# Optimization experiments

Measured on AMD Instinct MI355X. Metric: run time of the kernel, lower is better.

## Reference

```python
import jax, jax.numpy as jnp
import numpy as np

EPS = 1e-5

def mish(x):
    return x * jnp.tanh(jnp.logaddexp(x, 0.0))

def instance_norm(x, gamma, beta):
    # x: (N, C, D, H, W); normalize per (N, C) over spatial dims
    mu = jnp.mean(x, axis=(2, 3, 4), keepdims=True)
    var = jnp.var(x, axis=(2, 3, 4), keepdims=True)
    xh = (x - mu) * jax.lax.rsqrt(var + EPS)
    return xh * gamma[None, :, None, None, None] + beta[None, :, None, None, None]

def conv3d(x, w, stride, padding):
    return jax.lax.conv_general_dilated(
        x, w, window_strides=(stride, stride, stride), padding=padding,
        dimension_numbers=('NCDHW', 'OIDHW', 'NCDHW'))

def pad_k(k, p):
    # center-pad kernel spatial dims up to 5x5x5
    return jnp.pad(k, ((0, 0), (0, 0), (p, p), (p, p), (p, p)))

def mode_conv(x, t, c5, c3, c1, a3, a5, gw, gb, gamma, beta):
    N = x.shape[0]
    Co = c5.shape[0]
    # gate: Linear(num_tasks -> 5*Co), softmax over the 5 experts
    g = jax.nn.softmax((t @ gw.T + gb).reshape(N, 5, Co), axis=1)  # (N,5,Co)
    pool3 = jnp.full((3, 3, 3), 1.0 / 27.0, x.dtype)
    pool5 = jnp.full((5, 5, 5), 1.0 / 125.0, x.dtype)
    experts = jnp.stack([
        c5,                      # conv5x5
        pad_k(c3, 1),            # conv3x3 padded to 5
        pad_k(c1, 2),            # conv1x1 padded to 5
        pad_k(a3 * pool3, 1),    # avg3x3: (Co,Ci,1,1,1)*(3,3,3) broadcast, padded
        a5 * pool5,              # avg5x5
    ], axis=0)                   # (5, Co, Ci, 5, 5, 5)
    # per-sample synthesized kernel
    w = jnp.einsum('eoidhw,neo->noidhw', experts, g)  # (N, Co, Ci, 5,5,5)
    # per-sample conv3d, padding 'same' (training branch of original)
    y = jax.vmap(lambda xi, wi: conv3d(xi[None], wi, 1, 'SAME')[0])(x, w)
    return mish(instance_norm(y, gamma, beta))

def setup_inputs() -> dict:
    key = jax.random.key(0)
    ks = jax.random.split(key, 32)
    N, Ci, Co, T = 2, 32, 64, 10
    D = H = W = 64
    f32 = jnp.float32
    def kconv(k, co, ci, ksz, fan):
        bound = float(np.sqrt(6.0 / ((1.0 + 5.0) * fan)))  # kaiming_uniform a=sqrt(5), fan_out
        return jax.random.uniform(k, (co, ci, ksz, ksz, ksz), f32, -bound, bound)
    inp = {}
    inp['x'] = jax.random.normal(ks[0], (N, Ci, D, H, W), f32)
    inp['t'] = jax.random.normal(ks[1], (N, T), f32)
    def layer(base, ci, co):
        p = {}
        p['conv5'] = kconv(ks[base + 0], co, ci, 5, co * 125)
        p['conv3'] = kconv(ks[base + 1], co, ci, 3, co * 27)
        p['conv1'] = kconv(ks[base + 2], co, ci, 1, co)
        p['avg3'] = kconv(ks[base + 3], co, ci, 1, co)
        p['avg5'] = kconv(ks[base + 4], co, ci, 1, co)
        gb_bound = 1.0 / np.sqrt(T)
        p['gw'] = jax.random.uniform(ks[base + 5], (5 * co, T), f32, -gb_bound, gb_bound)
        p['gb'] = jax.random.uniform(ks[base + 6], (5 * co,), f32, -gb_bound, gb_bound)
        p['gamma'] = jnp.ones((co,), f32)
        p['beta'] = jnp.zeros((co,), f32)
        return p
    for name, v in layer(2, Ci, Co).items():
        inp['l1_' + name] = v
    for name, v in layer(12, Co, Co).items():
        inp['l2_' + name] = v
    dw_bound = float(np.sqrt(1.0 / (Co * 8)))
    inp['down_w'] = jax.random.uniform(ks[25], (Co, Co, 2, 2, 2), f32, -dw_bound, dw_bound)
    inp['down_gamma'] = jnp.ones((Co,), f32)
    inp['down_beta'] = jnp.zeros((Co,), f32)
    return inp

def reference(x, t,
              l1_conv5, l1_conv3, l1_conv1, l1_avg3, l1_avg5, l1_gw, l1_gb, l1_gamma, l1_beta,
              l2_conv5, l2_conv3, l2_conv1, l2_avg3, l2_avg5, l2_gw, l2_gb, l2_gamma, l2_beta,
              down_w, down_gamma, down_beta):
    h = mode_conv(x, t, l1_conv5, l1_conv3, l1_conv1, l1_avg3, l1_avg5, l1_gw, l1_gb, l1_gamma, l1_beta)
    x_skip = mode_conv(h, t, l2_conv5, l2_conv3, l2_conv1, l2_avg3, l2_avg5, l2_gw, l2_gb, l2_gamma, l2_beta)
    y = conv3d(x_skip, down_w, 2, 'VALID')
    y = mish(instance_norm(y, down_gamma, down_beta))
    return (y, x_skip)
```

## Files before the change

kernel.cpp:

```cpp
#include <hip/hip_runtime.h>
#include <cstdint>
#include <cstddef>

constexpr int NB  = 2;
constexpr int CO  = 64;
constexpr int DIM = 64;
constexpr int SP  = DIM * DIM * DIM;
constexpr int NC  = NB * CO;
constexpr int Y_SZ = NB * CO * 32 * 32 * 32;

typedef float f32x4 __attribute__((ext_vector_type(4)));
typedef short s16x8 __attribute__((ext_vector_type(8)));

__device__ __forceinline__ unsigned short f2bf(float f) {
    unsigned int u = __float_as_uint(f);
    unsigned int r = (u + 0x7fffu + ((u >> 16) & 1u)) >> 16;
    return (unsigned short)r;
}
__device__ __forceinline__ float bf2f(unsigned short u) {
    return __uint_as_float((unsigned int)u << 16);
}
__device__ __forceinline__ unsigned int pack2(float a, float b) {
    return (unsigned int)f2bf(a) | ((unsigned int)f2bf(b) << 16);
}
__device__ __forceinline__ float mish_f(float x) {
    float e = __expf(x);
    float num = e * (e + 2.f);
    float r = x * num * __builtin_amdgcn_rcpf(num + 2.f);
    return (x > 15.f) ? x : r;
}

__device__ __forceinline__ void gload_lds16(const void* g, void* l) {
    __builtin_amdgcn_global_load_lds(
        (const __attribute__((address_space(1))) unsigned int*)g,
        (__attribute__((address_space(3))) unsigned int*)l, 16, 0, 0);
}

__global__ void gate2_kernel(const float* __restrict__ t,
                             const float* __restrict__ gw1, const float* __restrict__ gb1,
                             float* __restrict__ g1,
                             const float* __restrict__ gw2, const float* __restrict__ gb2,
                             float* __restrict__ g2,
                             float* __restrict__ zbuf) {
    int tid = threadIdx.x;
    if (tid < 64) zbuf[tid] = 0.f;
    int layer = tid >> 7;
    int lt = tid & 127;
    int n = lt >> 6, co = lt & 63;
    const float* gw = layer ? gw2 : gw1;
    const float* gb = layer ? gb2 : gb1;
    float* g = layer ? g2 : g1;
    float tl[10];
#pragma unroll
    for (int k = 0; k < 10; ++k) tl[k] = t[n * 10 + k];
    float l[5];
#pragma unroll
    for (int e = 0; e < 5; ++e) {
        int row = e * CO + co;
        float acc = gb[row];
#pragma unroll
        for (int k = 0; k < 10; ++k) acc += tl[k] * gw[row * 10 + k];
        l[e] = acc;
    }
    float m = l[0];
#pragma unroll
    for (int e = 1; e < 5; ++e) m = fmaxf(m, l[e]);
    float s = 0.f;
#pragma unroll
    for (int e = 0; e < 5; ++e) { l[e] = expf(l[e] - m); s += l[e]; }
    float inv = 1.f / s;
#pragma unroll
    for (int e = 0; e < 5; ++e) g[(n * 5 + e) * CO + co] = l[e] * inv;
}

template <int CI>
__device__ __forceinline__ void synth_one(int idx, const float* __restrict__ g,
                                          const float* __restrict__ c5, const float* __restrict__ c3,
                                          const float* __restrict__ c1, const float* __restrict__ a3,
                                          const float* __restrict__ a5,
                                          unsigned short* __restrict__ wbuf) {
    int tap = idx % 125;
    int ci  = (idx / 125) % CI;
    int co  = (idx / (125 * CI)) % CO;
    int n   = idx / (125 * CI * CO);
    const float* gn = g + n * 5 * CO;
    float g0 = gn[0 * CO + co], g1 = gn[1 * CO + co], g2 = gn[2 * CO + co],
          g3 = gn[3 * CO + co], g4 = gn[4 * CO + co];
    int dz = tap / 25, dy = (tap / 5) % 5, dx = tap % 5;
    int oc = co * CI + ci;
    float v = g0 * c5[(size_t)oc * 125 + tap] + g4 * a5[oc] * (1.f / 125.f);
    if (dz >= 1 && dz <= 3 && dy >= 1 && dy <= 3 && dx >= 1 && dx <= 3)
        v += g1 * c3[(size_t)oc * 27 + (dz - 1) * 9 + (dy - 1) * 3 + (dx - 1)]
           + g3 * a3[oc] * (1.f / 27.f);
    if (dz == 2 && dy == 2 && dx == 2) v += g2 * c1[oc];
    int t = (dy * 5 + dx);
    int cich = ci >> 5, cil = ci & 31;
    wbuf[((((size_t)(n * 5 + dz) * (CI / 32) + cich) * 25 + t) * 64 + co) * 32 + cil] = f2bf(v);
}

__global__ void synth2_kernel(const float* __restrict__ g1,
                              const float* __restrict__ c51, const float* __restrict__ c31,
                              const float* __restrict__ c11, const float* __restrict__ a31,
                              const float* __restrict__ a51, unsigned short* __restrict__ w1,
                              const float* __restrict__ g2,
                              const float* __restrict__ c52, const float* __restrict__ c32,
                              const float* __restrict__ c12, const float* __restrict__ a32,
                              const float* __restrict__ a52, unsigned short* __restrict__ w2) {
    constexpr int T1 = NB * CO * 32 * 125;
    constexpr int T2 = NB * CO * 64 * 125;
    int idx = blockIdx.x * 256 + threadIdx.x;
    if (idx < T1)
        synth_one<32>(idx, g1, c51, c31, c11, a31, a51, w1);
    else if (idx < T1 + T2)
        synth_one<64>(idx - T1, g2, c52, c32, c12, a32, a52, w2);
}

__global__ __launch_bounds__(256) void x_to_cl(const float* __restrict__ x,
                                               unsigned short* __restrict__ xcl) {
    __shared__ float ld[32][256];
    int b = blockIdx.x;
    int n = b >> 10;
    size_t base = (size_t)(b & 1023) * 256;
    int tid = threadIdx.x;
    const float* xp = x + (size_t)n * 32 * SP + base + tid;
#pragma unroll
    for (int c = 0; c < 32; ++c) ld[c][tid] = xp[(size_t)c * SP];
    __syncthreads();
    uint4* op = (uint4*)(xcl + ((size_t)n * SP + base) * 32);
#pragma unroll
    for (int r = 0; r < 4; ++r) {
        int idx = r * 256 + tid;
        int px = idx >> 2, q = idx & 3;
        uint4 o;
        o.x = pack2(ld[q * 8 + 0][px], ld[q * 8 + 1][px]);
        o.y = pack2(ld[q * 8 + 2][px], ld[q * 8 + 3][px]);
        o.z = pack2(ld[q * 8 + 4][px], ld[q * 8 + 5][px]);
        o.w = pack2(ld[q * 8 + 6][px], ld[q * 8 + 7][px]);
        op[idx] = o;
    }
}

template <int CI, int PCH, bool OUT_G8>
__global__ __launch_bounds__(512, 4) void conv5_mfma(const unsigned short* __restrict__ xin,
                                                     const unsigned short* __restrict__ wbuf,
                                                     unsigned short* __restrict__ outp,
                                                     float* __restrict__ part,
                                                     const void* __restrict__ zbuf) {
    constexpr int NCH = CI / 32;
    constexpr int NS  = 5 * NCH;
    __shared__ __align__(16) unsigned short lds[2][12800];

    const int bid = blockIdx.x;
    const int b   = (bid & 7) * 256 + (bid >> 3);
    const int xt  = b & 3;
    const int yt  = (b >> 2) & 3;
    const int z   = (b >> 4) & 63;
    const int n   = b >> 10;
    const int tid = threadIdx.x;
    const int lane = tid & 63, wv = tid >> 6;
    const int xl = lane & 15, kh = lane >> 4;
    const int yh = wv >> 2, cq = wv & 3;

    f32x4 acc[8];
#pragma unroll
    for (int pt = 0; pt < 8; ++pt)
#pragma unroll
        for (int j = 0; j < 4; ++j) acc[pt][j] = 0.f;

    long goff[4]; int gval[4];
#pragma unroll
    for (int r = 0; r < 4; ++r) {
        int idx = tid + r * 512;
        int p = idx >> 2, khs = idx & 3;
        int xx = p % 20, yy = p / 20;
        int yi = yt * 16 - 2 + yy, xi = xt * 16 - 2 + xx;
        gval[r] = ((unsigned)yi < 64u) && ((unsigned)xi < 64u);
        goff[r] = ((long)(yi * 64 + xi) * CI + khs * 8) * 2;
    }

    auto stage = [&](int s, int buf) {
        int dz = s / NCH, cich = s % NCH;
        int zi = z + dz - 2;
        bool zok = (unsigned)zi < 64u;
        const char* pb = (const char*)xin
                       + ((size_t)(n * SP + zi * 4096) * CI + cich * 32) * 2;
        char* lb = (char*)&lds[buf][0];
#pragma unroll
        for (int r = 0; r < 4; ++r) {
            int idx = tid + r * 512;
            if (idx < 1600) {
                const void* g = (zok && gval[r]) ? (const void*)(pb + goff[r]) : zbuf;
                gload_lds16(g, lb + idx * 16);
            }
        }
    };

    auto compute = [&](int s, int buf) {
        int dz = s / NCH, cich = s % NCH;
        const unsigned short* wp = wbuf
            + ((size_t)((n * 5 + dz) * NCH + cich) * 25) * 2048
            + cq * 512 + xl * 32 + kh * 8;
        const char* src = (const char*)&lds[buf][0];
        __builtin_amdgcn_s_setprio(1);
#pragma unroll 1
        for (int dx = 0; dx < 5; ++dx) {
            int xx = xl + dx;
            s16x8 fr[12];
#pragma unroll
            for (int r = 0; r < 12; ++r) {
                int row = yh * 8 + r;
                fr[r] = *(const s16x8*)(src + (size_t)(row * 20 + xx) * 64 + kh * 16);
            }
#pragma unroll
            for (int dy = 0; dy < 5; ++dy) {
                s16x8 a = *(const s16x8*)(wp + (size_t)(dy * 5 + dx) * 2048);
#pragma unroll
                for (int pt = 0; pt < 8; ++pt)
                    acc[pt] = __builtin_amdgcn_mfma_f32_16x16x32_bf16(
                        a, fr[pt + dy], acc[pt], 0, 0, 0);
            }
        }
        __builtin_amdgcn_s_setprio(0);
    };

    stage(0, 0);
    __syncthreads();
#pragma unroll 1
    for (int s = 0; s < NS; ++s) {
        if (s + 1 < NS) stage(s + 1, (s + 1) & 1);
        compute(s, s & 1);
        __syncthreads();
    }

    {
        float s1[4], s2[4];
#pragma unroll
        for (int j = 0; j < 4; ++j) { s1[j] = 0.f; s2[j] = 0.f; }
#pragma unroll
        for (int pt = 0; pt < 8; ++pt)
#pragma unroll
            for (int j = 0; j < 4; ++j) {
                float v = acc[pt][j];
                s1[j] += v; s2[j] += v * v;
            }
#pragma unroll
        for (int o = 1; o < 16; o <<= 1)
#pragma unroll
            for (int j = 0; j < 4; ++j) {
                s1[j] += __shfl_xor(s1[j], o, 64);
                s2[j] += __shfl_xor(s2[j], o, 64);
            }
        if (xl == 0) {
            int co = cq * 16 + kh * 4;
            int cb = (b & 1023) * 2 + yh;
#pragma unroll
            for (int j = 0; j < 4; ++j) {
                part[((size_t)(n * 2 + 0) * 64 + co + j) * PCH + cb] = s1[j];
                part[((size_t)(n * 2 + 1) * 64 + co + j) * PCH + cb] = s2[j];
            }
        }
    }

    {
        char* tb = (char*)&lds[0][0];
#pragma unroll
        for (int pt = 0; pt < 8; ++pt) {
            int pix = (yh * 8 + pt) * 16 + xl;
            unsigned int ad = ((unsigned)(pix * 128 + cq * 32 + kh * 8))
                              ^ ((unsigned)(pix & 7) << 4);
            *(unsigned int*)(tb + ad)     = pack2(acc[pt][0], acc[pt][1]);
            *(unsigned int*)(tb + ad + 4) = pack2(acc[pt][2], acc[pt][3]);
        }
        __syncthreads();
#pragma unroll
        for (int it = 0; it < 4; ++it) {
            int idx = it * 512 + tid;
            int pix = idx >> 3, ch = idx & 7;
            uint4 v = *(const uint4*)(tb + (((unsigned)idx * 16)
                                            ^ ((unsigned)(pix & 7) << 4)));
            int y = yt * 16 + (pix >> 4), x = xt * 16 + (pix & 15);
            size_t zyx = (size_t)z * 4096 + y * 64 + x;
            if (OUT_G8)
                *(uint4*)(outp + ((size_t)(n * 8 + ch) * SP + zyx) * 8) = v;
            else
                *(uint4*)(outp + ((size_t)n * SP + zyx) * 64 + ch * 8) = v;
        }
    }
}

template <int CH>
__global__ void stats_fin(const float* __restrict__ part, float* __restrict__ st,
                          float invS) {
    int blk = blockIdx.x;
    int n = blk >> 6, co = blk & 63;
    int tid = threadIdx.x;
    const float* ps = part + ((size_t)(n * 2 + 0) * 64 + co) * CH;
    const float* pq = part + ((size_t)(n * 2 + 1) * 64 + co) * CH;
    float s1 = 0.f, s2 = 0.f;
    for (int i = tid; i < CH; i += 256) { s1 += ps[i]; s2 += pq[i]; }
#pragma unroll
    for (int o = 1; o < 64; o <<= 1) {
        s1 += __shfl_xor(s1, o, 64);
        s2 += __shfl_xor(s2, o, 64);
    }
    __shared__ float sh1[4], sh2[4];
    if ((tid & 63) == 0) { sh1[tid >> 6] = s1; sh2[tid >> 6] = s2; }
    __syncthreads();
    if (tid == 0) {
        float a = sh1[0] + sh1[1] + sh1[2] + sh1[3];
        float q = sh2[0] + sh2[1] + sh2[2] + sh2[3];
        float mean = a * invS;
        float var  = q * invS - mean * mean;
        st[(n * 64 + co) * 2]     = mean;
        st[(n * 64 + co) * 2 + 1] = rsqrtf(var + 1e-5f);
    }
}

__global__ void norm_mish_cl_kernel(unsigned short* __restrict__ h,
                                    const float* __restrict__ st,
                                    const float* __restrict__ gamma,
                                    const float* __restrict__ beta) {
    size_t idx = (size_t)blockIdx.x * 256 + threadIdx.x;
    uint4 v = ((uint4*)h)[idx];
    int c0 = ((int)(idx & 7)) * 8;
    size_t pix = idx >> 3;
    int n = (int)(pix >> 18);
    unsigned int* pv = &v.x;
#pragma unroll
    for (int q = 0; q < 4; ++q) {
        unsigned int wv = pv[q];
        unsigned int out = 0;
#pragma unroll
        for (int hv = 0; hv < 2; ++hv) {
            int c = c0 + 2 * q + hv;
            int nc = n * 64 + c;
            float val = bf2f((unsigned short)((wv >> (16 * hv)) & 0xffffu));
            float xh = (val - st[nc * 2]) * st[nc * 2 + 1] * gamma[c] + beta[c];
            out |= ((unsigned int)f2bf(mish_f(xh))) << (16 * hv);
        }
        pv[q] = out;
    }
    ((uint4*)h)[idx] = v;
}

template <int SHIFT>
__global__ void norm_mish_kernel(float* __restrict__ buf, const float* __restrict__ stats,
                                 const float* __restrict__ gamma, const float* __restrict__ beta,
                                 int total4) {
    int idx = blockIdx.x * 256 + threadIdx.x;
    if (idx >= total4) return;
    float4 v = reinterpret_cast<float4*>(buf)[idx];
    int nc = idx >> (SHIFT - 2);
    int c  = nc & 63;
    float mean = stats[nc * 2], inv = stats[nc * 2 + 1];
    float ga = gamma[c], be = beta[c];
    float* pv = &v.x;
#pragma unroll
    for (int k = 0; k < 4; ++k) {
        float xh = (pv[k] - mean) * inv * ga + be;
        pv[k] = mish_f(xh);
    }
    reinterpret_cast<float4*>(buf)[idx] = v;
}

__global__ __launch_bounds__(256) void down_conv_kernel(const unsigned short* __restrict__ h3,
                                                        const float* __restrict__ dw,
                                                        const float* __restrict__ st,
                                                        const float* __restrict__ gamma,
                                                        const float* __restrict__ beta,
                                                        float* __restrict__ xskip,
                                                        float* __restrict__ out,
                                                        float* __restrict__ part) {
    __shared__ float ls[8][2][8][64];
    int b   = blockIdx.x;
    int yt  = b & 7;
    int z   = (b >> 3) & 31;
    int n   = b >> 8;
    int tid = threadIdx.x;
    int xo  = tid & 31;
    int cog = tid >> 5;

    float acc[4][8];
#pragma unroll
    for (int yo = 0; yo < 4; ++yo)
#pragma unroll
        for (int j = 0; j < 8; ++j) acc[yo][j] = 0.f;

    for (int cc = 0; cc < 8; ++cc) {
#pragma unroll
        for (int r = 0; r < 4; ++r) {
            int p  = r * 256 + tid;
            int xx = p & 63, yy = (p >> 6) & 7, dz = p >> 9;
            int zi = 2 * z + dz, yi = yt * 8 + yy;
            size_t zyx = (size_t)zi * 4096 + yi * 64 + xx;
            uint4 v = *(const uint4*)(h3 + ((size_t)(n * 8 + cc) * SP + zyx) * 8);
            unsigned int* pv = &v.x;
#pragma unroll
            for (int q = 0; q < 4; ++q) {
#pragma unroll
                for (int hv = 0; hv < 2; ++hv) {
                    int c  = 2 * q + hv;
                    int ci = cc * 8 + c;
                    int nc = n * 64 + ci;
                    float val = bf2f((unsigned short)((pv[q] >> (16 * hv)) & 0xffffu));
                    float nv  = mish_f((val - st[nc * 2]) * st[nc * 2 + 1] * gamma[ci]
                                       + beta[ci]);
                    ls[c][dz][yy][xx] = nv;
                    xskip[((size_t)(n * CO + ci) * 64 + zi) * 4096 + yi * 64 + xx] = nv;
                }
            }
        }
        __syncthreads();
#pragma unroll 1
        for (int c = 0; c < 8; ++c) {
            int ci = cc * 8 + c;
#pragma unroll
            for (int tap = 0; tap < 8; ++tap) {
                int dz = tap >> 2, dy = (tap >> 1) & 1, dx = tap & 1;
                float w[8];
#pragma unroll
                for (int j = 0; j < 8; ++j)
                    w[j] = dw[((size_t)(cog * 8 + j) * CO + ci) * 8 + tap];
#pragma unroll
                for (int yo = 0; yo < 4; ++yo) {
                    float xv = ls[c][dz][yo * 2 + dy][2 * xo + dx];
#pragma unroll
                    for (int j = 0; j < 8; ++j) acc[yo][j] += w[j] * xv;
                }
            }
        }
        __syncthreads();
    }
#pragma unroll
    for (int yo = 0; yo < 4; ++yo)
#pragma unroll
        for (int j = 0; j < 8; ++j)
            out[((size_t)(n * CO + cog * 8 + j) * 32 + z) * 1024 + (yt * 4 + yo) * 32 + xo]
                = acc[yo][j];

    float s1[8], s2[8];
#pragma unroll
    for (int j = 0; j < 8; ++j) { s1[j] = 0.f; s2[j] = 0.f; }
#pragma unroll
    for (int yo = 0; yo < 4; ++yo)
#pragma unroll
        for (int j = 0; j < 8; ++j) {
            float v = acc[yo][j];
            s1[j] += v; s2[j] += v * v;
        }
#pragma unroll
    for (int o = 1; o < 32; o <<= 1)
#pragma unroll
        for (int j = 0; j < 8; ++j) {
            s1[j] += __shfl_xor(s1[j], o, 64);
            s2[j] += __shfl_xor(s2[j], o, 64);
        }
    if (xo == 0) {
        int cb = b & 255;
#pragma unroll
        for (int j = 0; j < 8; ++j) {
            int co = cog * 8 + j;
            part[((size_t)(n * 2 + 0) * 64 + co) * 256 + cb] = s1[j];
            part[((size_t)(n * 2 + 1) * 64 + co) * 256 + cb] = s2[j];
        }
    }
}

extern "C" void kernel_launch(void* const* d_in, const int* in_sizes, int n_in,
                              void* d_out, int out_size, void* d_ws, size_t ws_size,
                              hipStream_t stream) {
    const float* x      = (const float*)d_in[0];
    const float* t      = (const float*)d_in[1];
    const float* l1_c5  = (const float*)d_in[2];
    const float* l1_c3  = (const float*)d_in[3];
    const float* l1_c1  = (const float*)d_in[4];
    const float* l1_a3  = (const float*)d_in[5];
    const float* l1_a5  = (const float*)d_in[6];
    const float* l1_gw  = (const float*)d_in[7];
    const float* l1_gb  = (const float*)d_in[8];
    const float* l1_ga  = (const float*)d_in[9];
    const float* l1_be  = (const float*)d_in[10];
    const float* l2_c5  = (const float*)d_in[11];
    const float* l2_c3  = (const float*)d_in[12];
    const float* l2_c1  = (const float*)d_in[13];
    const float* l2_a3  = (const float*)d_in[14];
    const float* l2_a5  = (const float*)d_in[15];
    const float* l2_gw  = (const float*)d_in[16];
    const float* l2_gb  = (const float*)d_in[17];
    const float* l2_ga  = (const float*)d_in[18];
    const float* l2_be  = (const float*)d_in[19];
    const float* down_w = (const float*)d_in[20];
    const float* dn_ga  = (const float*)d_in[21];
    const float* dn_be  = (const float*)d_in[22];

    char* ws = (char*)d_ws;
    unsigned short* xcl = (unsigned short*)(ws);
    unsigned short* h3  = (unsigned short*)(ws);
    float* part1 = (float*)(ws + 33554432);
    unsigned short* h2  = (unsigned short*)(ws + 67108864);
    unsigned short* w1  = (unsigned short*)(ws + 134217728);
    unsigned short* w2  = (unsigned short*)(ws + 135241728);
    float* part2 = (float*)(ws + 137289728);
    float* part3 = (float*)(ws + 139386880);
    float* g1    = (float*)(ws + 139649024);
    float* g2    = (float*)(ws + 139651584);
    float* st1   = (float*)(ws + 139654144);
    float* st2   = (float*)(ws + 139655168);
    float* st3   = (float*)(ws + 139656192);
    float* zbuf  = (float*)(ws + 139657216);

    float* yout  = (float*)d_out;
    float* xskip = (float*)d_out + Y_SZ;

    gate2_kernel<<<1, 256, 0, stream>>>(t, l1_gw, l1_gb, g1, l2_gw, l2_gb, g2, zbuf);
    synth2_kernel<<<6000, 256, 0, stream>>>(g1, l1_c5, l1_c3, l1_c1, l1_a3, l1_a5, w1,
                                            g2, l2_c5, l2_c3, l2_c1, l2_a3, l2_a5, w2);
    x_to_cl<<<2048, 256, 0, stream>>>(x, xcl);

    conv5_mfma<32, 2048, false><<<2048, 512, 0, stream>>>(xcl, w1, h2, part1, zbuf);
    stats_fin<2048><<<128, 256, 0, stream>>>(part1, st1, 1.f / SP);
    norm_mish_cl_kernel<<<16384, 256, 0, stream>>>(h2, st1, l1_ga, l1_be);

    conv5_mfma<64, 2048, true><<<2048, 512, 0, stream>>>(h2, w2, h3, part2, zbuf);
    stats_fin<2048><<<128, 256, 0, stream>>>(part2, st2, 1.f / SP);

    down_conv_kernel<<<NB * 32 * 8, 256, 0, stream>>>(h3, down_w, st2, l2_ga, l2_be,
                                                      xskip, yout, part3);
    stats_fin<256><<<128, 256, 0, stream>>>(part3, st3, 1.f / 32768.f);
    norm_mish_kernel<15><<<(NC * 32768 / 4 + 255) / 256, 256, 0, stream>>>(
        yout, st3, dn_ga, dn_be, NC * 32768 / 4);
}
```

Measured before the change: 758.4 us.

## Switch conv5 to 32x32x16 MFMA with 8x32 spatial tiles and LDS stats

Replaces the 16x16x32 bf16 MFMA conv with 32x32x16 MFMA tiles, changing the block's spatial tile from 16x16 to 8 rows by 32 columns and reorganizing the LDS staging layout and fragment loads to match. Each wave now computes 32 channels by 2 rows of 32 pixels, reducing fragment loads per MFMA and weight register traffic. Instance-norm partial statistics are now computed from the bf16-rounded values staged in LDS with a block-level reduction, giving one partial per block and halving the stats_fin input. The stats change rounding slightly and the larger LDS footprint may affect occupancy.

```diff
diff --git a/kernel.cpp b/kernel.cpp
--- a/kernel.cpp
+++ b/kernel.cpp
@@ -9,8 +9,9 @@
 constexpr int NC  = NB * CO;
 constexpr int Y_SZ = NB * CO * 32 * 32 * 32;
 
-typedef float f32x4 __attribute__((ext_vector_type(4)));
-typedef short s16x8 __attribute__((ext_vector_type(8)));
+typedef float f32x4  __attribute__((ext_vector_type(4)));
+typedef float f32x16 __attribute__((ext_vector_type(16)));
+typedef short s16x8  __attribute__((ext_vector_type(8)));
 
 __device__ __forceinline__ unsigned short f2bf(float f) {
     unsigned int u = __float_as_uint(f);
@@ -141,41 +142,43 @@
 }
 
 template <int CI, int PCH, bool OUT_G8>
-__global__ __launch_bounds__(512, 4) void conv5_mfma(const unsigned short* __restrict__ xin,
-                                                     const unsigned short* __restrict__ wbuf,
-                                                     unsigned short* __restrict__ outp,
-                                                     float* __restrict__ part,
-                                                     const void* __restrict__ zbuf) {
+__global__ __launch_bounds__(512, 4) void conv5_mfma32(const unsigned short* __restrict__ xin,
+                                                       const unsigned short* __restrict__ wbuf,
+                                                       unsigned short* __restrict__ outp,
+                                                       float* __restrict__ part,
+                                                       const void* __restrict__ zbuf) {
     constexpr int NCH = CI / 32;
     constexpr int NS  = 5 * NCH;
-    __shared__ __align__(16) unsigned short lds[2][12800];
+    __shared__ __align__(16) unsigned short lds[2][13824];
 
     const int bid = blockIdx.x;
     const int b   = (bid & 7) * 256 + (bid >> 3);
-    const int xt  = b & 3;
-    const int yt  = (b >> 2) & 3;
+    const int xt  = b & 1;
+    const int yt  = (b >> 1) & 7;
     const int z   = (b >> 4) & 63;
     const int n   = b >> 10;
     const int tid = threadIdx.x;
     const int lane = tid & 63, wv = tid >> 6;
-    const int xl = lane & 15, kh = lane >> 4;
-    const int yh = wv >> 2, cq = wv & 3;
-
-    f32x4 acc[8];
-#pragma unroll
-    for (int pt = 0; pt < 8; ++pt)
-#pragma unroll
-        for (int j = 0; j < 4; ++j) acc[pt][j] = 0.f;
+    const int l31 = lane & 31, kh = lane >> 5;
+    const int yp = wv >> 1, cq = wv & 1;
+
+    f32x16 acc[2];
+#pragma unroll
+    for (int sl = 0; sl < 2; ++sl)
+#pragma unroll
+        for (int j = 0; j < 16; ++j) acc[sl][j] = 0.f;
 
     long goff[4]; int gval[4];
 #pragma unroll
     for (int r = 0; r < 4; ++r) {
         int idx = tid + r * 512;
-        int p = idx >> 2, khs = idx & 3;
-        int xx = p % 20, yy = p / 20;
-        int yi = yt * 16 - 2 + yy, xi = xt * 16 - 2 + xx;
+        int xx = idx % 36;
+        int t2 = idx / 36;
+        int c  = t2 & 3;
+        int row = t2 >> 2;
+        int yi = yt * 8 - 2 + row, xi = xt * 32 - 2 + xx;
         gval[r] = ((unsigned)yi < 64u) && ((unsigned)xi < 64u);
-        goff[r] = ((long)(yi * 64 + xi) * CI + khs * 8) * 2;
+        goff[r] = ((long)(yi * 64 + xi) * CI + c * 8) * 2;
     }
 
     auto stage = [&](int s, int buf) {
@@ -188,7 +191,7 @@
 #pragma unroll
         for (int r = 0; r < 4; ++r) {
             int idx = tid + r * 512;
-            if (idx < 1600) {
+            if (idx < 1728) {
                 const void* g = (zok && gval[r]) ? (const void*)(pb + goff[r]) : zbuf;
                 gload_lds16(g, lb + idx * 16);
             }
@@ -197,28 +200,30 @@
 
     auto compute = [&](int s, int buf) {
         int dz = s / NCH, cich = s % NCH;
-        const unsigned short* wp = wbuf
+        const unsigned short* wpl = wbuf
             + ((size_t)((n * 5 + dz) * NCH + cich) * 25) * 2048
-            + cq * 512 + xl * 32 + kh * 8;
-        const char* src = (const char*)&lds[buf][0];
+            + (cq * 32 + l31) * 32 + kh * 8;
+        const char* bb = (const char*)&lds[buf][0] + kh * 576 + l31 * 16;
         __builtin_amdgcn_s_setprio(1);
 #pragma unroll 1
         for (int dx = 0; dx < 5; ++dx) {
-            int xx = xl + dx;
-            s16x8 fr[12];
-#pragma unroll
-            for (int r = 0; r < 12; ++r) {
-                int row = yh * 8 + r;
-                fr[r] = *(const s16x8*)(src + (size_t)(row * 20 + xx) * 64 + kh * 16);
-            }
-#pragma unroll
-            for (int dy = 0; dy < 5; ++dy) {
-                s16x8 a = *(const s16x8*)(wp + (size_t)(dy * 5 + dx) * 2048);
-#pragma unroll
-                for (int pt = 0; pt < 8; ++pt)
-                    acc[pt] = __builtin_amdgcn_mfma_f32_16x16x32_bf16(
-                        a, fr[pt + dy], acc[pt], 0, 0, 0);
-            }
+            s16x8 fr[6][2];
+#pragma unroll
+            for (int rr = 0; rr < 6; ++rr)
+#pragma unroll
+                for (int m = 0; m < 2; ++m)
+                    fr[rr][m] = *(const s16x8*)(bb
+                        + (size_t)(((yp * 2 + rr) * 4 + m * 2) * 576) + dx * 16);
+#pragma unroll
+            for (int dy = 0; dy < 5; ++dy)
+#pragma unroll
+                for (int m = 0; m < 2; ++m) {
+                    s16x8 a = *(const s16x8*)(wpl + (size_t)(dy * 5 + dx) * 2048 + m * 16);
+                    acc[0] = __builtin_amdgcn_mfma_f32_32x32x16_bf16(
+                        a, fr[dy][m], acc[0], 0, 0, 0);
+                    acc[1] = __builtin_amdgcn_mfma_f32_32x32x16_bf16(
+                        a, fr[dy + 1][m], acc[1], 0, 0, 0);
+                }
         }
         __builtin_amdgcn_s_setprio(0);
     };
@@ -232,59 +237,59 @@
         __syncthreads();
     }
 
+    char* tb = (char*)&lds[0][0];
+#pragma unroll
+    for (int yo = 0; yo < 2; ++yo) {
+        int px = (yp * 2 + yo) * 32 + l31;
+        unsigned int swz = (unsigned)(px & 7) << 4;
+#pragma unroll
+        for (int rp = 0; rp < 8; ++rp) {
+            int r0 = rp * 2;
+            int ch0 = (r0 & 3) + 8 * (r0 >> 2) + 4 * kh + cq * 32;
+            *(unsigned int*)(tb + (((unsigned)(px * 128 + ch0 * 2)) ^ swz)) =
+                pack2(acc[yo][r0], acc[yo][r0 + 1]);
+        }
+    }
+    __syncthreads();
+
+#pragma unroll
+    for (int it = 0; it < 4; ++it) {
+        int idx = it * 512 + tid;
+        int pix = idx >> 3, ch8 = idx & 7;
+        uint4 v = *(const uint4*)(tb + (((unsigned)idx * 16)
+                                        ^ ((unsigned)(pix & 7) << 4)));
+        int y = yt * 8 + (pix >> 5), x = xt * 32 + (pix & 31);
+        size_t zyx = (size_t)z * 4096 + y * 64 + x;
+        if (OUT_G8)
+            *(uint4*)(outp + ((size_t)(n * 8 + ch8) * SP + zyx) * 8) = v;
+        else
+            *(uint4*)(outp + ((size_t)n * SP + zyx) * 64 + ch8 * 8) = v;
+    }
+
     {
-        float s1[4], s2[4];
-#pragma unroll
-        for (int j = 0; j < 4; ++j) { s1[j] = 0.f; s2[j] = 0.f; }
-#pragma unroll
-        for (int pt = 0; pt < 8; ++pt)
-#pragma unroll
-            for (int j = 0; j < 4; ++j) {
-                float v = acc[pt][j];
-                s1[j] += v; s2[j] += v * v;
-            }
-#pragma unroll
-        for (int o = 1; o < 16; o <<= 1)
-#pragma unroll
-            for (int j = 0; j < 4; ++j) {
-                s1[j] += __shfl_xor(s1[j], o, 64);
-                s2[j] += __shfl_xor(s2[j], o, 64);
-            }
-        if (xl == 0) {
-            int co = cq * 16 + kh * 4;
-            int cb = (b & 1023) * 2 + yh;
-#pragma unroll
-            for (int j = 0; j < 4; ++j) {
-                part[((size_t)(n * 2 + 0) * 64 + co + j) * PCH + cb] = s1[j];
-                part[((size_t)(n * 2 + 1) * 64 + co + j) * PCH + cb] = s2[j];
-            }
-        }
-    }
-
-    {
-        char* tb = (char*)&lds[0][0];
-#pragma unroll
-        for (int pt = 0; pt < 8; ++pt) {
-            int pix = (yh * 8 + pt) * 16 + xl;
-            unsigned int ad = ((unsigned)(pix * 128 + cq * 32 + kh * 8))
-                              ^ ((unsigned)(pix & 7) << 4);
-            *(unsigned int*)(tb + ad)     = pack2(acc[pt][0], acc[pt][1]);
-            *(unsigned int*)(tb + ad + 4) = pack2(acc[pt][2], acc[pt][3]);
-        }
-        __syncthreads();
-#pragma unroll
-        for (int it = 0; it < 4; ++it) {
-            int idx = it * 512 + tid;
-            int pix = idx >> 3, ch = idx & 7;
-            uint4 v = *(const uint4*)(tb + (((unsigned)idx * 16)
-                                            ^ ((unsigned)(pix & 7) << 4)));
-            int y = yt * 16 + (pix >> 4), x = xt * 16 + (pix & 15);
-            size_t zyx = (size_t)z * 4096 + y * 64 + x;
-            if (OUT_G8)
-                *(uint4*)(outp + ((size_t)(n * 8 + ch) * SP + zyx) * 8) = v;
-            else
-                *(uint4*)(outp + ((size_t)n * SP + zyx) * 64 + ch * 8) = v;
-        }
+        int ch = tid & 63, g = tid >> 6;
+        float s1 = 0.f, s2 = 0.f;
+#pragma unroll 8
+        for (int j = 0; j < 32; ++j) {
+            int px = g * 32 + j;
+            unsigned short u = *(const unsigned short*)(tb
+                + (((unsigned)(px * 128 + ch * 2)) ^ ((unsigned)(px & 7) << 4)));
+            float v = bf2f(u);
+            s1 += v; s2 += v * v;
+        }
+        float* sh1 = (float*)(tb + 36864);
+        float* sh2 = sh1 + 512;
+        sh1[g * 64 + ch] = s1;
+        sh2[g * 64 + ch] = s2;
+    }
+    __syncthreads();
+    if (tid < 128) {
+        int co = tid & 63, si = tid >> 6;
+        const float* shp = (float*)(tb + 36864) + si * 512;
+        float v = 0.f;
+#pragma unroll
+        for (int g = 0; g < 8; ++g) v += shp[g * 64 + co];
+        part[((size_t)(n * 2 + si) * 64 + co) * PCH + (b & 1023)] = v;
     }
 }
 
@@ -517,12 +522,12 @@
                                             g2, l2_c5, l2_c3, l2_c1, l2_a3, l2_a5, w2);
     x_to_cl<<<2048, 256, 0, stream>>>(x, xcl);
 
-    conv5_mfma<32, 2048, false><<<2048, 512, 0, stream>>>(xcl, w1, h2, part1, zbuf);
-    stats_fin<2048><<<128, 256, 0, stream>>>(part1, st1, 1.f / SP);
+    conv5_mfma32<32, 1024, false><<<2048, 512, 0, stream>>>(xcl, w1, h2, part1, zbuf);
+    stats_fin<1024><<<128, 256, 0, stream>>>(part1, st1, 1.f / SP);
     norm_mish_cl_kernel<<<16384, 256, 0, stream>>>(h2, st1, l1_ga, l1_be);
 
-    conv5_mfma<64, 2048, true><<<2048, 512, 0, stream>>>(h2, w2, h3, part2, zbuf);
-    stats_fin<2048><<<128, 256, 0, stream>>>(part2, st2, 1.f / SP);
+    conv5_mfma32<64, 1024, true><<<2048, 512, 0, stream>>>(h2, w2, h3, part2, zbuf);
+    stats_fin<1024><<<128, 256, 0, stream>>>(part2, st2, 1.f / SP);
 
     down_conv_kernel<<<NB * 32 * 8, 256, 0, stream>>>(h3, down_w, st2, l2_ga, l2_be,
                                                       xskip, yout, part3);
```

Result: slower. 969.7 us (+27.9%).
